# Kernel optimization log

Measured on AMD Instinct MI355X. Metric: run time of the kernel, lower is better.

Reference implementation:

```python
import jax, jax.numpy as jnp
import numpy as np

N = 100000
E = 1600000
C_IN = 128
C_OUT = 128
BN_EPS = 1e-5


def setup_inputs() -> dict:
    key = jax.random.key(0)
    k1, k2, k3, k4 = jax.random.split(key, 4)
    x = jax.random.normal(k1, (N, C_IN), dtype=jnp.float32)
    edge_index = jax.random.randint(k2, (2, E), 0, N, dtype=jnp.int64)
    edge_weight = jax.random.uniform(k3, (E,), dtype=jnp.float32)
    W = jax.random.normal(k4, (C_IN, C_OUT), dtype=jnp.float32) / np.sqrt(C_IN)
    gamma = jnp.ones((C_OUT,), dtype=jnp.float32)
    beta = jnp.zeros((C_OUT,), dtype=jnp.float32)
    return {"x": x, "edge_index": edge_index, "edge_weight": edge_weight,
            "W": W, "gamma": gamma, "beta": beta}


def reference(x, edge_index, edge_weight, W, gamma, beta):
    n = x.shape[0]
    row, col = edge_index[0], edge_index[1]  # messages flow row -> col
    loop = jnp.arange(n, dtype=edge_index.dtype)
    # GCNConv (improved=False): add self-loops with weight 1
    row_f = jnp.concatenate([row, loop])
    col_f = jnp.concatenate([col, loop])
    w_f = jnp.concatenate([edge_weight, jnp.ones((n,), x.dtype)])
    # symmetric normalization: D^{-1/2} A D^{-1/2}
    deg = jax.ops.segment_sum(w_f, col_f, num_segments=n)
    deg_safe = jnp.where(deg > 0, deg, 1.0)
    dis = jnp.where(deg > 0, jax.lax.rsqrt(deg_safe), 0.0)
    norm = dis[row_f] * w_f * dis[col_f]  # [E+N]
    # linear transform then scatter-add aggregation (bias=False)
    h = x @ W  # [N, C_out]
    agg = jax.ops.segment_sum(h[row_f] * norm[:, None], col_f, num_segments=n)
    # BatchNorm1d (training mode: batch stats, biased variance) + ReLU
    mean = agg.mean(axis=0)
    var = agg.var(axis=0)
    y = (agg - mean) * jax.lax.rsqrt(var + BN_EPS) * gamma + beta
    return jax.nn.relu(y)
```

## Files before the change

kernel.cpp:

```cpp
#include <hip/hip_runtime.h>

#define C 128
#define MAXNB 1024
typedef unsigned int uint;
typedef unsigned short ushort;
typedef __attribute__((ext_vector_type(4))) float f32x4;
typedef __attribute__((ext_vector_type(8))) short bf16x8;

__device__ __forceinline__ float blo(uint u) { return __uint_as_float(u << 16); }
__device__ __forceinline__ float bhi(uint u) { return __uint_as_float(u & 0xFFFF0000u); }
#define PACKBF(LO, HI) __builtin_amdgcn_perm(__float_as_uint(HI) + 0x8000u, \
                                             __float_as_uint(LO) + 0x8000u, 0x07060302u)

__global__ __launch_bounds__(512) void k_hist(const int* __restrict__ col,
                                              int* __restrict__ counts,
                                              int nE, int NB, int NBLK) {
    __shared__ int hist[MAXNB];
    const int t = threadIdx.x, blk = blockIdx.x;
    for (int i = t; i < NB; i += 512) hist[i] = 0;
    __syncthreads();
    const int base = blk * 8192;
    for (int k = 0; k < 16; ++k) {
        int e = base + k * 512 + t;
        if (e < nE) atomicAdd(&hist[col[e] >> 7], 1);
    }
    __syncthreads();
    for (int i = t; i < NB; i += 512) counts[i * NBLK + blk] = hist[i];
}

__global__ __launch_bounds__(256) void k_scan1(int* __restrict__ counts,
                                               int* __restrict__ bsum, int scanN) {
    __shared__ int s[256];
    int t = threadIdx.x;
    int i = blockIdx.x * 256 + t;
    int v = (i < scanN) ? counts[i] : 0;
    s[t] = v;
    __syncthreads();
    for (int d = 1; d < 256; d <<= 1) {
        int a = (t >= d) ? s[t - d] : 0;
        __syncthreads();
        s[t] += a;
        __syncthreads();
    }
    if (i < scanN) counts[i] = s[t] - v;
    if (t == 255) bsum[blockIdx.x] = s[255];
}

__global__ __launch_bounds__(256) void k_scan2(int* __restrict__ bsum, int nb) {
    __shared__ int s[256];
    __shared__ int carry;
    int t = threadIdx.x;
    if (t == 0) carry = 0;
    __syncthreads();
    int nch = (nb + 255) / 256;
    for (int c = 0; c < nch; ++c) {
        int i = c * 256 + t;
        int v = (i < nb) ? bsum[i] : 0;
        s[t] = v;
        __syncthreads();
        for (int d = 1; d < 256; d <<= 1) {
            int a = (t >= d) ? s[t - d] : 0;
            __syncthreads();
            s[t] += a;
            __syncthreads();
        }
        int cb = carry;
        if (i < nb) bsum[i] = s[t] - v + cb;
        int tot = s[255];
        __syncthreads();
        if (t == 0) carry = cb + tot;
        __syncthreads();
    }
}

__global__ __launch_bounds__(512) void k_scatter(const int* __restrict__ ei,
                                                 const float* __restrict__ ew,
                                                 const int* __restrict__ counts,
                                                 const int* __restrict__ bsum,
                                                 int2* __restrict__ ev2,
                                                 int nE, int NB, int NBLK) {
    __shared__ int base_l[MAXNB];
    __shared__ int cnt_l[MAXNB];
    const int t = threadIdx.x, blk = blockIdx.x;
    for (int i = t; i < NB; i += 512) {
        int idx = i * NBLK + blk;
        base_l[i] = counts[idx] + bsum[idx >> 8];
        cnt_l[i] = 0;
    }
    __syncthreads();
    const int base = blk * 8192;
    for (int k = 0; k < 16; ++k) {
        int e = base + k * 512 + t;
        if (e >= nE) continue;
        int c = ei[nE + e];
        int row = ei[e];
        int b = c >> 7;
        int pos = base_l[b] + atomicAdd(&cnt_l[b], 1);
        ev2[pos] = make_int2(((c & 127) << 25) | row, __float_as_int(ew[e]));
    }
}

__global__ __launch_bounds__(256) void k_sortdeg(const int2* __restrict__ ev2,
                                                 const int* __restrict__ counts,
                                                 const int* __restrict__ bsum,
                                                 int2* __restrict__ evs,
                                                 int* __restrict__ offs,
                                                 float* __restrict__ dis,
                                                 int n, int nE, int NB, int NBLK) {
    __shared__ int cnt[128];
    __shared__ float wsum[128];
    __shared__ int cur[128];
    __shared__ int sc[128];
    __shared__ int seg[2];
    const int t = threadIdx.x, b = blockIdx.x;
    if (t < 128) { cnt[t] = 0; wsum[t] = 0.f; }
    if (t == 0) {
        int i0 = b * NBLK;
        seg[0] = counts[i0] + bsum[i0 >> 8];
    } else if (t == 1) {
        int i1 = (b + 1) * NBLK;
        seg[1] = (b + 1 < NB) ? counts[i1] + bsum[i1 >> 8] : nE;
    }
    __syncthreads();
    const int s = seg[0], e = seg[1];
    for (int i = s + t; i < e; i += 256) {
        int2 E = ev2[i];
        int cl = (uint)E.x >> 25;
        atomicAdd(&cnt[cl], 1);
        atomicAdd(&wsum[cl], __int_as_float(E.y));
    }
    __syncthreads();
    if (t < 128) sc[t] = cnt[t];
    __syncthreads();
    for (int d = 1; d < 128; d <<= 1) {
        int v = 0;
        if (t < 128 && t >= d) v = sc[t - d];
        __syncthreads();
        if (t < 128) sc[t] += v;
        __syncthreads();
    }
    if (t < 128) {
        int col = (b << 7) + t;
        int base = s + sc[t] - cnt[t];
        cur[t] = base;
        if (col < n) {
            offs[col] = base;
            dis[col] = rsqrtf(1.0f + wsum[t]);
        }
    }
    if (b == 0 && t == 0) offs[n] = nE;
    __syncthreads();
    for (int i = s + t; i < e; i += 256) {
        int2 E = ev2[i];
        int cl = (uint)E.x >> 25;
        int pos = atomicAdd(&cur[cl], 1);
        evs[pos] = make_int2(E.x & 0x1FFFFFF, E.y);
    }
}

__global__ __launch_bounds__(256) void k_cvt(const float4* __restrict__ x4,
                                             const float* __restrict__ dis,
                                             ushort4* __restrict__ xb4,
                                             const float* __restrict__ W,
                                             ushort* __restrict__ WbT,
                                             long total4, int cvtB) {
    if ((int)blockIdx.x >= cvtB) {
        int idx = ((int)blockIdx.x - cvtB) * 256 + threadIdx.x;
        int k = idx >> 7, o = idx & 127;
        uint u = __float_as_uint(W[idx]);
        WbT[o * 128 + k] = (ushort)((u + 0x7FFFu + ((u >> 16) & 1u)) >> 16);
        return;
    }
    long i = (long)blockIdx.x * 256 + threadIdx.x;
    if (i >= total4) return;
    float d = dis[i >> 5];
    float4 v = x4[i];
    ushort4 r;
#define RNE(OUT, F)                                                     \
    {                                                                   \
        uint u = __float_as_uint((F) * d);                              \
        OUT = (ushort)((u + 0x7FFFu + ((u >> 16) & 1u)) >> 16);         \
    }
    RNE(r.x, v.x) RNE(r.y, v.y) RNE(r.z, v.z) RNE(r.w, v.w)
#undef RNE
    xb4[i] = r;
}

__global__ __launch_bounds__(256) void k_segagg(const ushort* __restrict__ xb,
                                                const int2* __restrict__ ev,
                                                const int* __restrict__ offs,
                                                const float* __restrict__ dis,
                                                ushort* __restrict__ aggb, int n) {
    const int lane = threadIdx.x & 15;
    const int sub  = threadIdx.x >> 4;
    const int col  = blockIdx.x * 16 + sub;
    if (col >= n) return;

    uint4 sv = *(const uint4*)(xb + (size_t)col * C + lane * 8);
    float acc[8] = {blo(sv.x), bhi(sv.x), blo(sv.y), bhi(sv.y),
                    blo(sv.z), bhi(sv.z), blo(sv.w), bhi(sv.w)};

    int i = offs[col];
    const int end = offs[col + 1];

#define EDGE(E, V)                                                        \
    {                                                                     \
        float nw = __int_as_float(E.y);                                   \
        acc[0] = fmaf(nw, blo(V.x), acc[0]);                              \
        acc[1] = fmaf(nw, bhi(V.x), acc[1]);                              \
        acc[2] = fmaf(nw, blo(V.y), acc[2]);                              \
        acc[3] = fmaf(nw, bhi(V.y), acc[3]);                              \
        acc[4] = fmaf(nw, blo(V.z), acc[4]);                              \
        acc[5] = fmaf(nw, bhi(V.z), acc[5]);                              \
        acc[6] = fmaf(nw, blo(V.w), acc[6]);                              \
        acc[7] = fmaf(nw, bhi(V.w), acc[7]);                              \
    }
#define GATH(K) uint4 v##K = *(const uint4*)(xb + (size_t)e##K.x * C + lane * 8);

    for (; i + 8 <= end; i += 8) {
        int2 e0 = ev[i],     e1 = ev[i + 1], e2 = ev[i + 2], e3 = ev[i + 3];
        int2 e4 = ev[i + 4], e5 = ev[i + 5], e6 = ev[i + 6], e7 = ev[i + 7];
        GATH(0) GATH(1) GATH(2) GATH(3) GATH(4) GATH(5) GATH(6) GATH(7)
        EDGE(e0, v0) EDGE(e1, v1) EDGE(e2, v2) EDGE(e3, v3)
        EDGE(e4, v4) EDGE(e5, v5) EDGE(e6, v6) EDGE(e7, v7)
    }
    for (; i + 2 <= end; i += 2) {
        int2 e0 = ev[i], e1 = ev[i + 1];
        GATH(0) GATH(1)
        EDGE(e0, v0) EDGE(e1, v1)
    }
    if (i < end) {
        int2 e0 = ev[i];
        GATH(0)
        EDGE(e0, v0)
    }
#undef GATH
#undef EDGE

    float d = dis[col];
    uint4 r;
    r.x = PACKBF(d * acc[0], d * acc[1]);
    r.y = PACKBF(d * acc[2], d * acc[3]);
    r.z = PACKBF(d * acc[4], d * acc[5]);
    r.w = PACKBF(d * acc[6], d * acc[7]);
    *(uint4*)(aggb + (size_t)col * C + lane * 8) = r;
}

__global__ __launch_bounds__(256, 4) void k_gemm(const ushort* __restrict__ aggb,
                                                 ushort* __restrict__ outb,
                                                 const ushort* __restrict__ WbT,
                                                 int n) {
    const int t = threadIdx.x;
    const int lane = t & 63;
    const int wv = t >> 6;
    const int lr = lane & 15;
    const int lk = lane >> 4;
    const long m = (long)blockIdx.x * 64 + wv * 16 + lr;
    const bool inr = m < (long)n;

    bf16x8 b0, b1, b2, b3;
    if (inr) {
        const bf16x8* p = (const bf16x8*)(aggb + (size_t)m * C + lk * 8);
        b0 = p[0];
        b1 = p[4];
        b2 = p[8];
        b3 = p[12];
    } else {
        b0 = b1 = b2 = b3 = (bf16x8){0, 0, 0, 0, 0, 0, 0, 0};
    }

    f32x4 acc[8];
#pragma unroll
    for (int ot = 0; ot < 8; ++ot) acc[ot] = (f32x4){0.f, 0.f, 0.f, 0.f};

#pragma unroll 2
    for (int ot = 0; ot < 8; ++ot) {
        const ushort* wp = WbT + (ot * 16 + lr) * 128 + lk * 8;
        bf16x8 a0 = *(const bf16x8*)(wp);
        bf16x8 a1 = *(const bf16x8*)(wp + 32);
        bf16x8 a2 = *(const bf16x8*)(wp + 64);
        bf16x8 a3 = *(const bf16x8*)(wp + 96);
        acc[ot] = __builtin_amdgcn_mfma_f32_16x16x32_bf16(a0, b0, acc[ot], 0, 0, 0);
        acc[ot] = __builtin_amdgcn_mfma_f32_16x16x32_bf16(a1, b1, acc[ot], 0, 0, 0);
        acc[ot] = __builtin_amdgcn_mfma_f32_16x16x32_bf16(a2, b2, acc[ot], 0, 0, 0);
        acc[ot] = __builtin_amdgcn_mfma_f32_16x16x32_bf16(a3, b3, acc[ot], 0, 0, 0);
    }

    if (inr) {
        ushort* orow = outb + (size_t)m * C + lk * 4;
#pragma unroll
        for (int ot = 0; ot < 8; ++ot) {
            uint2 r;
            r.x = PACKBF(acc[ot][0], acc[ot][1]);
            r.y = PACKBF(acc[ot][2], acc[ot][3]);
            *(uint2*)(orow + ot * 16) = r;
        }
    }
}

__global__ __launch_bounds__(1024) void k_stats(const uint4* __restrict__ ob4,
                                                float* __restrict__ part, int n) {
    const int t = threadIdx.x;
    const int cg = t & 15;
    const int rl = t >> 4;
    float s[8] = {0, 0, 0, 0, 0, 0, 0, 0};
    float q[8] = {0, 0, 0, 0, 0, 0, 0, 0};
    for (int r = blockIdx.x * 64 + rl; r < n; r += gridDim.x * 64) {
        uint4 v = ob4[(size_t)r * 16 + cg];
        float f0 = blo(v.x), f1 = bhi(v.x), f2 = blo(v.y), f3 = bhi(v.y);
        float f4 = blo(v.z), f5 = bhi(v.z), f6 = blo(v.w), f7 = bhi(v.w);
        s[0] += f0; q[0] = fmaf(f0, f0, q[0]);
        s[1] += f1; q[1] = fmaf(f1, f1, q[1]);
        s[2] += f2; q[2] = fmaf(f2, f2, q[2]);
        s[3] += f3; q[3] = fmaf(f3, f3, q[3]);
        s[4] += f4; q[4] = fmaf(f4, f4, q[4]);
        s[5] += f5; q[5] = fmaf(f5, f5, q[5]);
        s[6] += f6; q[6] = fmaf(f6, f6, q[6]);
        s[7] += f7; q[7] = fmaf(f7, f7, q[7]);
    }
#pragma unroll
    for (int j = 0; j < 8; ++j) {
        s[j] += __shfl_xor(s[j], 16); s[j] += __shfl_xor(s[j], 32);
        q[j] += __shfl_xor(q[j], 16); q[j] += __shfl_xor(q[j], 32);
    }
    __shared__ float lds_s[16][128];
    __shared__ float lds_q[16][128];
    const int wvi = t >> 6;
    if ((t & 63) < 16) {
#pragma unroll
        for (int j = 0; j < 8; ++j) {
            lds_s[wvi][cg * 8 + j] = s[j];
            lds_q[wvi][cg * 8 + j] = q[j];
        }
    }
    __syncthreads();
    if (t < 128) {
        float ps = 0.f;
#pragma unroll
        for (int w = 0; w < 16; ++w) ps += lds_s[w][t];
        part[(size_t)blockIdx.x * 256 + t] = ps;
    } else if (t < 256) {
        int c = t - 128;
        float pq = 0.f;
#pragma unroll
        for (int w = 0; w < 16; ++w) pq += lds_q[w][c];
        part[(size_t)blockIdx.x * 256 + t] = pq;
    }
}

__global__ __launch_bounds__(256) void k_finish(const float* __restrict__ part,
                                                float* __restrict__ sums, int nblk) {
    int t = threadIdx.x;
    float s = 0.f;
    for (int b = blockIdx.x; b < nblk; b += gridDim.x) s += part[(size_t)b * 256 + t];
    atomicAdd(&sums[t], s);
}

__global__ __launch_bounds__(256) void k_apply(const uint4* __restrict__ ob4,
                                               float* __restrict__ out,
                                               const float* __restrict__ sums,
                                               const float* __restrict__ gamma,
                                               const float* __restrict__ beta,
                                               int n) {
    size_t idx = (size_t)blockIdx.x * 256 + threadIdx.x;
    size_t total = (size_t)n * 16;
    if (idx >= total) return;
    int cg = (int)(idx & 15);
    int c0 = cg * 8;
    float inv_n = 1.0f / (float)n;
    uint4 v = ob4[idx];
    float f[8] = {blo(v.x), bhi(v.x), blo(v.y), bhi(v.y),
                  blo(v.z), bhi(v.z), blo(v.w), bhi(v.w)};
    float4 r0, r1;
#define BN1(OUT, J)                                                        \
    {                                                                      \
        float mean = sums[c0 + J] * inv_n;                                 \
        float var  = fmaxf(sums[C + c0 + J] * inv_n - mean * mean, 0.f);   \
        float sc   = rsqrtf(var + 1e-5f) * gamma[c0 + J];                  \
        OUT = fmaxf(fmaf(f[J] - mean, sc, beta[c0 + J]), 0.f);             \
    }
    BN1(r0.x, 0) BN1(r0.y, 1) BN1(r0.z, 2) BN1(r0.w, 3)
    BN1(r1.x, 4) BN1(r1.y, 5) BN1(r1.z, 6) BN1(r1.w, 7)
#undef BN1
    float4* orow = (float4*)(out + (idx >> 4) * C + c0);
    orow[0] = r0;
    orow[1] = r1;
}

extern "C" void kernel_launch(void* const* d_in, const int* in_sizes, int n_in,
                              void* d_out, int out_size, void* d_ws, size_t ws_size,
                              hipStream_t stream) {
    const float* x     = (const float*)d_in[0];
    const int*   ei    = (const int*)d_in[1];
    const float* ew    = (const float*)d_in[2];
    const float* W     = (const float*)d_in[3];
    const float* gamma = (const float*)d_in[4];
    const float* beta  = (const float*)d_in[5];

    const int n  = in_sizes[0] / C;
    const int nE = in_sizes[2];

    const int NB    = (n + 127) >> 7;
    const int NBLK  = (nE + 8191) / 8192;
    const int scanN = NB * NBLK;
    const int scanB = (scanN + 255) / 256;
    const int SB    = 256;

    float* out = (float*)d_out;
    char* p = (char*)d_ws;
#define ALLOC(TYPE, NAME, BYTES) \
    TYPE NAME = (TYPE)p; p += ((size_t)(BYTES) + 255) & ~(size_t)255;
    ALLOC(int2*,   ev2,    (size_t)nE * 8)
    ALLOC(int2*,   evs,    (size_t)nE * 8)
    ALLOC(ushort*, xb,     (size_t)n * C * 2)
    ALLOC(ushort*, aggb,   (size_t)n * C * 2)
    ALLOC(ushort*, outb,   (size_t)n * C * 2)
    ALLOC(int*,    counts, (size_t)scanN * 4)
    ALLOC(int*,    bsum,   (size_t)scanB * 4)
    ALLOC(float*,  dis,    (size_t)n * 4)
    ALLOC(int*,    offs,   (size_t)(n + 1) * 4)
    ALLOC(ushort*, WbT,    32768)
    ALLOC(float*,  sums,   1024)
    ALLOC(float*,  part,   (size_t)SB * 256 * 4)
#undef ALLOC

    const long total4 = (long)n * 32;
    const long totalb = (long)n * 16;
    const int  cvtB   = (int)((total4 + 255) / 256);

    hipMemsetAsync(sums, 0, 256 * 4, stream);

    k_hist   <<<NBLK, 512, 0, stream>>>(ei + nE, counts, nE, NB, NBLK);
    k_scan1  <<<scanB, 256, 0, stream>>>(counts, bsum, scanN);
    k_scan2  <<<1, 256, 0, stream>>>(bsum, scanB);
    k_scatter<<<NBLK, 512, 0, stream>>>(ei, ew, counts, bsum, ev2, nE, NB, NBLK);
    k_sortdeg<<<NB, 256, 0, stream>>>(ev2, counts, bsum, evs, offs, dis, n, nE, NB, NBLK);
    k_cvt    <<<cvtB + 64, 256, 0, stream>>>((const float4*)x, dis, (ushort4*)xb, W, WbT, total4, cvtB);
    k_segagg <<<(n + 15) / 16, 256, 0, stream>>>(xb, evs, offs, dis, aggb, n);
    k_gemm   <<<(n + 63) / 64, 256, 0, stream>>>(aggb, outb, WbT, n);
    k_stats  <<<SB, 1024, 0, stream>>>((const uint4*)outb, part, n);
    k_finish <<<16, 256, 0, stream>>>(part, sums, SB);
    k_apply  <<<(int)((totalb + 255) / 256), 256, 0, stream>>>((const uint4*)outb, out, sums, gamma, beta, n);
}
```

Before: 198.9 us.

## Fuse per-bucket column sort into segment aggregation via shared-memory edge staging

The separate sort pass, which wrote column-sorted edges and offsets to global memory, is removed. k_segagg now loads each 128-column bucket's edges into shared memory, counting-sorts them there, and aggregates 8 columns per 16-lane group. A reduced k_deg kernel keeps only the degree computation. This removes one global write and read of the edge array plus a kernel launch. In exchange the aggregation grid shrinks from about 6250 to about 782 blocks, and buckets with more than 4096 edges fall back to a slow linear scan.

```diff
diff --git a/kernel.cpp b/kernel.cpp
--- a/kernel.cpp
+++ b/kernel.cpp
@@ -2,6 +2,7 @@
 
 #define C 128
 #define MAXNB 1024
+#define CAP 4096
 typedef unsigned int uint;
 typedef unsigned short ushort;
 typedef __attribute__((ext_vector_type(4))) float f32x4;
@@ -100,62 +101,26 @@
     }
 }
 
-__global__ __launch_bounds__(256) void k_sortdeg(const int2* __restrict__ ev2,
-                                                 const int* __restrict__ counts,
-                                                 const int* __restrict__ bsum,
-                                                 int2* __restrict__ evs,
-                                                 int* __restrict__ offs,
-                                                 float* __restrict__ dis,
-                                                 int n, int nE, int NB, int NBLK) {
-    __shared__ int cnt[128];
+__global__ __launch_bounds__(256) void k_deg(const int2* __restrict__ ev2,
+                                             const int* __restrict__ counts,
+                                             const int* __restrict__ bsum,
+                                             float* __restrict__ dis,
+                                             int n, int nE, int NB, int NBLK) {
     __shared__ float wsum[128];
-    __shared__ int cur[128];
-    __shared__ int sc[128];
     __shared__ int seg[2];
     const int t = threadIdx.x, b = blockIdx.x;
-    if (t < 128) { cnt[t] = 0; wsum[t] = 0.f; }
-    if (t == 0) {
-        int i0 = b * NBLK;
-        seg[0] = counts[i0] + bsum[i0 >> 8];
-    } else if (t == 1) {
-        int i1 = (b + 1) * NBLK;
-        seg[1] = (b + 1 < NB) ? counts[i1] + bsum[i1 >> 8] : nE;
-    }
+    if (t < 128) wsum[t] = 0.f;
+    if (t == 0) { int i0 = b * NBLK; seg[0] = counts[i0] + bsum[i0 >> 8]; }
+    if (t == 1) { int i1 = (b + 1) * NBLK; seg[1] = (b + 1 < NB) ? counts[i1] + bsum[i1 >> 8] : nE; }
     __syncthreads();
     const int s = seg[0], e = seg[1];
     for (int i = s + t; i < e; i += 256) {
         int2 E = ev2[i];
-        int cl = (uint)E.x >> 25;
-        atomicAdd(&cnt[cl], 1);
-        atomicAdd(&wsum[cl], __int_as_float(E.y));
-    }
-    __syncthreads();
-    if (t < 128) sc[t] = cnt[t];
-    __syncthreads();
-    for (int d = 1; d < 128; d <<= 1) {
-        int v = 0;
-        if (t < 128 && t >= d) v = sc[t - d];
-        __syncthreads();
-        if (t < 128) sc[t] += v;
-        __syncthreads();
-    }
-    if (t < 128) {
-        int col = (b << 7) + t;
-        int base = s + sc[t] - cnt[t];
-        cur[t] = base;
-        if (col < n) {
-            offs[col] = base;
-            dis[col] = rsqrtf(1.0f + wsum[t]);
-        }
-    }
-    if (b == 0 && t == 0) offs[n] = nE;
-    __syncthreads();
-    for (int i = s + t; i < e; i += 256) {
-        int2 E = ev2[i];
-        int cl = (uint)E.x >> 25;
-        int pos = atomicAdd(&cur[cl], 1);
-        evs[pos] = make_int2(E.x & 0x1FFFFFF, E.y);
-    }
+        atomicAdd(&wsum[(uint)E.x >> 25], __int_as_float(E.y));
+    }
+    __syncthreads();
+    int col = (b << 7) + t;
+    if (t < 128 && col < n) dis[col] = rsqrtf(1.0f + wsum[t]);
 }
 
 __global__ __launch_bounds__(256) void k_cvt(const float4* __restrict__ x4,
@@ -187,21 +152,63 @@
 }
 
 __global__ __launch_bounds__(256) void k_segagg(const ushort* __restrict__ xb,
-                                                const int2* __restrict__ ev,
-                                                const int* __restrict__ offs,
+                                                const int2* __restrict__ ev2,
+                                                const int* __restrict__ counts,
+                                                const int* __restrict__ bsum,
                                                 const float* __restrict__ dis,
-                                                ushort* __restrict__ aggb, int n) {
-    const int lane = threadIdx.x & 15;
-    const int sub  = threadIdx.x >> 4;
-    const int col  = blockIdx.x * 16 + sub;
-    if (col >= n) return;
-
-    uint4 sv = *(const uint4*)(xb + (size_t)col * C + lane * 8);
-    float acc[8] = {blo(sv.x), bhi(sv.x), blo(sv.y), bhi(sv.y),
-                    blo(sv.z), bhi(sv.z), blo(sv.w), bhi(sv.w)};
-
-    int i = offs[col];
-    const int end = offs[col + 1];
+                                                ushort* __restrict__ aggb,
+                                                int n, int nE, int NB, int NBLK) {
+    __shared__ int2 se[CAP];
+    __shared__ int cnt[128];
+    __shared__ int sc[128];
+    __shared__ int cur[128];
+    __shared__ int seg[2];
+    const int t = threadIdx.x, b = blockIdx.x;
+    if (t < 128) cnt[t] = 0;
+    if (t == 0) { int i0 = b * NBLK; seg[0] = counts[i0] + bsum[i0 >> 8]; }
+    if (t == 1) { int i1 = (b + 1) * NBLK; seg[1] = (b + 1 < NB) ? counts[i1] + bsum[i1 >> 8] : nE; }
+    __syncthreads();
+    const int s = seg[0], e = seg[1];
+    const int m = e - s;
+    const bool fits = (m <= CAP);
+
+    if (fits) {
+        int2 held[16];
+#pragma unroll
+        for (int r = 0; r < 16; ++r) {
+            int idx = r * 256 + t;
+            held[r] = make_int2(0, 0);
+            if (idx < m) {
+                held[r] = ev2[s + idx];
+                atomicAdd(&cnt[(uint)held[r].x >> 25], 1);
+            }
+        }
+        __syncthreads();
+        if (t < 128) sc[t] = cnt[t];
+        __syncthreads();
+        for (int d = 1; d < 128; d <<= 1) {
+            int v = 0;
+            if (t < 128 && t >= d) v = sc[t - d];
+            __syncthreads();
+            if (t < 128) sc[t] += v;
+            __syncthreads();
+        }
+        if (t < 128) cur[t] = sc[t] - cnt[t];
+        __syncthreads();
+#pragma unroll
+        for (int r = 0; r < 16; ++r) {
+            int idx = r * 256 + t;
+            if (idx < m) {
+                int cl = (uint)held[r].x >> 25;
+                int pos = atomicAdd(&cur[cl], 1);
+                se[pos] = make_int2(held[r].x & 0x1FFFFFF, held[r].y);
+            }
+        }
+        __syncthreads();
+    }
+
+    const int lane = t & 15;
+    const int g = t >> 4;
 
 #define EDGE(E, V)                                                        \
     {                                                                     \
@@ -217,33 +224,56 @@
     }
 #define GATH(K) uint4 v##K = *(const uint4*)(xb + (size_t)e##K.x * C + lane * 8);
 
-    for (; i + 8 <= end; i += 8) {
-        int2 e0 = ev[i],     e1 = ev[i + 1], e2 = ev[i + 2], e3 = ev[i + 3];
-        int2 e4 = ev[i + 4], e5 = ev[i + 5], e6 = ev[i + 6], e7 = ev[i + 7];
-        GATH(0) GATH(1) GATH(2) GATH(3) GATH(4) GATH(5) GATH(6) GATH(7)
-        EDGE(e0, v0) EDGE(e1, v1) EDGE(e2, v2) EDGE(e3, v3)
-        EDGE(e4, v4) EDGE(e5, v5) EDGE(e6, v6) EDGE(e7, v7)
-    }
-    for (; i + 2 <= end; i += 2) {
-        int2 e0 = ev[i], e1 = ev[i + 1];
-        GATH(0) GATH(1)
-        EDGE(e0, v0) EDGE(e1, v1)
-    }
-    if (i < end) {
-        int2 e0 = ev[i];
-        GATH(0)
-        EDGE(e0, v0)
+    for (int cc = 0; cc < 8; ++cc) {
+        const int cl = g * 8 + cc;
+        const int col = (b << 7) + cl;
+        if (col >= n) continue;
+
+        uint4 sv = *(const uint4*)(xb + (size_t)col * C + lane * 8);
+        float acc[8] = {blo(sv.x), bhi(sv.x), blo(sv.y), bhi(sv.y),
+                        blo(sv.z), bhi(sv.z), blo(sv.w), bhi(sv.w)};
+
+        if (fits) {
+            int i = sc[cl] - cnt[cl];
+            const int end2 = sc[cl];
+            for (; i + 8 <= end2; i += 8) {
+                int2 e0 = se[i],     e1 = se[i + 1], e2 = se[i + 2], e3 = se[i + 3];
+                int2 e4 = se[i + 4], e5 = se[i + 5], e6 = se[i + 6], e7 = se[i + 7];
+                GATH(0) GATH(1) GATH(2) GATH(3) GATH(4) GATH(5) GATH(6) GATH(7)
+                EDGE(e0, v0) EDGE(e1, v1) EDGE(e2, v2) EDGE(e3, v3)
+                EDGE(e4, v4) EDGE(e5, v5) EDGE(e6, v6) EDGE(e7, v7)
+            }
+            for (; i + 2 <= end2; i += 2) {
+                int2 e0 = se[i], e1 = se[i + 1];
+                GATH(0) GATH(1)
+                EDGE(e0, v0) EDGE(e1, v1)
+            }
+            if (i < end2) {
+                int2 e0 = se[i];
+                GATH(0)
+                EDGE(e0, v0)
+            }
+        } else {
+            for (int i = s; i < e; ++i) {
+                int2 E = ev2[i];
+                if ((int)((uint)E.x >> 25) == cl) {
+                    int2 e0 = make_int2(E.x & 0x1FFFFFF, E.y);
+                    GATH(0)
+                    EDGE(e0, v0)
+                }
+            }
+        }
+
+        float d = dis[col];
+        uint4 r;
+        r.x = PACKBF(d * acc[0], d * acc[1]);
+        r.y = PACKBF(d * acc[2], d * acc[3]);
+        r.z = PACKBF(d * acc[4], d * acc[5]);
+        r.w = PACKBF(d * acc[6], d * acc[7]);
+        *(uint4*)(aggb + (size_t)col * C + lane * 8) = r;
     }
 #undef GATH
 #undef EDGE
-
-    float d = dis[col];
-    uint4 r;
-    r.x = PACKBF(d * acc[0], d * acc[1]);
-    r.y = PACKBF(d * acc[2], d * acc[3]);
-    r.z = PACKBF(d * acc[4], d * acc[5]);
-    r.w = PACKBF(d * acc[6], d * acc[7]);
-    *(uint4*)(aggb + (size_t)col * C + lane * 8) = r;
 }
 
 __global__ __launch_bounds__(256, 4) void k_gemm(const ushort* __restrict__ aggb,
@@ -411,14 +441,12 @@
 #define ALLOC(TYPE, NAME, BYTES) \
     TYPE NAME = (TYPE)p; p += ((size_t)(BYTES) + 255) & ~(size_t)255;
     ALLOC(int2*,   ev2,    (size_t)nE * 8)
-    ALLOC(int2*,   evs,    (size_t)nE * 8)
     ALLOC(ushort*, xb,     (size_t)n * C * 2)
     ALLOC(ushort*, aggb,   (size_t)n * C * 2)
     ALLOC(ushort*, outb,   (size_t)n * C * 2)
     ALLOC(int*,    counts, (size_t)scanN * 4)
     ALLOC(int*,    bsum,   (size_t)scanB * 4)
     ALLOC(float*,  dis,    (size_t)n * 4)
-    ALLOC(int*,    offs,   (size_t)(n + 1) * 4)
     ALLOC(ushort*, WbT,    32768)
     ALLOC(float*,  sums,   1024)
     ALLOC(float*,  part,   (size_t)SB * 256 * 4)
@@ -434,9 +462,9 @@
     k_scan1  <<<scanB, 256, 0, stream>>>(counts, bsum, scanN);
     k_scan2  <<<1, 256, 0, stream>>>(bsum, scanB);
     k_scatter<<<NBLK, 512, 0, stream>>>(ei, ew, counts, bsum, ev2, nE, NB, NBLK);
-    k_sortdeg<<<NB, 256, 0, stream>>>(ev2, counts, bsum, evs, offs, dis, n, nE, NB, NBLK);
+    k_deg    <<<NB, 256, 0, stream>>>(ev2, counts, bsum, dis, n, nE, NB, NBLK);
     k_cvt    <<<cvtB + 64, 256, 0, stream>>>((const float4*)x, dis, (ushort4*)xb, W, WbT, total4, cvtB);
-    k_segagg <<<(n + 15) / 16, 256, 0, stream>>>(xb, evs, offs, dis, aggb, n);
+    k_segagg <<<NB, 256, 0, stream>>>(xb, ev2, counts, bsum, dis, aggb, n, nE, NB, NBLK);
     k_gemm   <<<(n + 63) / 64, 256, 0, stream>>>(aggb, outb, WbT, n);
     k_stats  <<<SB, 1024, 0, stream>>>((const uint4*)outb, part, n);
     k_finish <<<16, 256, 0, stream>>>(part, sums, SB);
```

Measured after the change: 194.4 us, median of 3. -2.2%, faster.
